# Performance work log

Measured on AMD Instinct MI355X. Metric: run time of the kernel, lower is better.

Reference implementation:

```python
import jax, jax.numpy as jnp
import numpy as np

N_NODES = 50000
N_EDGES = 1600000
NEG_SLOPE = 0.2


def _gat_layer(x, src, dst, W, a_src, a_dst, b, n_nodes):
    # PyG GATConv (heads=1, concat=True): h = xW; e_ij = LeakyReLU(a_src.h_j + a_dst.h_i)
    # alpha = softmax over incoming edges of each target i; out_i = sum_j alpha_ij h_j + b
    h = x @ W                                   # [N, out]
    alpha_src = h @ a_src                        # [N]
    alpha_dst = h @ a_dst                        # [N]
    e = alpha_src[src] + alpha_dst[dst]          # [E]
    e = jnp.where(e > 0, e, NEG_SLOPE * e)       # leaky_relu(0.2)
    m = jax.ops.segment_max(e, dst, num_segments=n_nodes)   # per-target max
    ex = jnp.exp(e - m[dst])
    denom = jax.ops.segment_sum(ex, dst, num_segments=n_nodes)
    alpha = ex / (denom[dst] + 1e-16)            # [E]
    out = jax.ops.segment_sum(alpha[:, None] * h[src], dst, num_segments=n_nodes)
    return out + b


def setup_inputs() -> dict:
    key = jax.random.key(0)
    ks = jax.random.split(key, 16)
    hid, out_dim, in_dim = 128, 5, 13
    x = jax.random.normal(ks[0], (N_NODES, in_dim), dtype=jnp.float32)
    edge_index = jax.random.randint(ks[1], (2, N_EDGES), 0, N_NODES, dtype=jnp.int64)
    s = 0.1
    return {
        "x": x,
        "edge_index": edge_index,
        "W1": jax.random.normal(ks[2], (in_dim, hid), dtype=jnp.float32) * s,
        "a_src1": jax.random.normal(ks[3], (hid,), dtype=jnp.float32) * s,
        "a_dst1": jax.random.normal(ks[4], (hid,), dtype=jnp.float32) * s,
        "b1": jnp.zeros((hid,), dtype=jnp.float32),
        "W2": jax.random.normal(ks[5], (hid, hid), dtype=jnp.float32) * s,
        "a_src2": jax.random.normal(ks[6], (hid,), dtype=jnp.float32) * s,
        "a_dst2": jax.random.normal(ks[7], (hid,), dtype=jnp.float32) * s,
        "b2": jnp.zeros((hid,), dtype=jnp.float32),
        "W3": jax.random.normal(ks[8], (hid, out_dim), dtype=jnp.float32) * s,
        "a_src3": jax.random.normal(ks[9], (out_dim,), dtype=jnp.float32) * s,
        "a_dst3": jax.random.normal(ks[10], (out_dim,), dtype=jnp.float32) * s,
        "b3": jnp.zeros((out_dim,), dtype=jnp.float32),
    }


def reference(x, edge_index, W1, a_src1, a_dst1, b1, W2, a_src2, a_dst2, b2,
              W3, a_src3, a_dst3, b3):
    n = x.shape[0]
    # GATConv add_self_loops=True: append (i, i) edges
    loops = jnp.arange(n, dtype=edge_index.dtype)
    src = jnp.concatenate([edge_index[0], loops])
    dst = jnp.concatenate([edge_index[1], loops])
    h = _gat_layer(x, src, dst, W1, a_src1, a_dst1, b1, n)
    h = jax.nn.relu(h)  # dropout identity in eval mode
    h = _gat_layer(h, src, dst, W2, a_src2, a_dst2, b2, n)
    h = jax.nn.relu(h)
    h = _gat_layer(h, src, dst, W3, a_src3, a_dst3, b3, n)
    return jax.nn.log_softmax(h, axis=1)
```

## Files before the change

### kernel.cpp

```cpp
#include <hip/hip_runtime.h>
#include <hip/hip_bf16.h>


#define LEAKY(e) ((e) > 0.f ? (e) : 0.2f * (e))
__device__ inline float clamp30(float e) { return fminf(fmaxf(e, -30.f), 30.f); }
__device__ inline float expc(float e) { return __expf(clamp30(LEAKY(e))); }

__device__ inline float ldany(const void* p, int bf, int i) {
    return bf ? __bfloat162float(((const __hip_bfloat16*)p)[i])
              : ((const float*)p)[i];
}
__device__ inline int ldidx(const void* p, int i64, long long i) {
    return i64 ? (int)(((const unsigned int*)p)[2 * i])
               : ((const int*)p)[i];
}

__device__ inline float bflo(unsigned int w) { return __uint_as_float(w << 16); }
__device__ inline float bfhi(unsigned int w) { return __uint_as_float(w & 0xffff0000u); }
__device__ inline unsigned short bfbits(float a) {
    __hip_bfloat16 x = __float2bfloat16(a);
    unsigned short u; __builtin_memcpy(&u, &x, 2); return u;
}
__device__ inline unsigned int packbf(float a, float b) {
    return (unsigned int)bfbits(a) | ((unsigned int)bfbits(b) << 16);
}

typedef __attribute__((ext_vector_type(8))) short short8;
typedef __attribute__((ext_vector_type(4))) float f32x4;

__global__ void detect_kernel(const void* W1, const void* ei, int* flags) {
    if (threadIdx.x == 0 && blockIdx.x == 0) {
        const unsigned int* w = (const unsigned int*)W1;
        int c = 0;
        for (int i = 0; i < 64; i++) {
            unsigned int e = (w[i] >> 7) & 0xFFu;
            if (e >= 0x70u && e <= 0x7Fu) c++;
        }
        flags[0] = (c >= 32) ? 1 : 0;
        const unsigned int* q = (const unsigned int*)ei;
        int z = 0;
        for (int i = 0; i < 64; i++)
            if (q[2 * i + 1] == 0u) z++;
        flags[1] = (z >= 32) ? 1 : 0;
    }
}


__global__ __launch_bounds__(256) void sortA_hist(
    const void* __restrict__ ei, const int* __restrict__ flags,
    int* __restrict__ blockHist, int E, int NBUK)
{
    __shared__ int hist[512];
    const int i64 = flags[1];
    const int tid = threadIdx.x, blk = blockIdx.x;
    for (int i = tid; i < NBUK; i += 256) hist[i] = 0;
    __syncthreads();
    const int chunk = (E + 255) / 256;
    const int e0 = blk * chunk, e1 = min(e0 + chunk, E);
    for (int t = e0 + tid; t < e1; t += 256) {
        int d = ldidx(ei, i64, (long long)E + t);
        atomicAdd(&hist[d >> 7], 1);
    }
    __syncthreads();
    for (int i = tid; i < NBUK; i += 256)
        blockHist[blk * NBUK + i] = hist[i];
}

__global__ __launch_bounds__(256) void sortB_prefix(
    int* __restrict__ blockHist, int* __restrict__ bucketBase, int NBUK)
{
    __shared__ int wt[4];
    __shared__ int wbase[4];
    const int b = blockIdx.x;
    const int tid = threadIdx.x, lane = tid & 63, wid = tid >> 6;
    int v = blockHist[tid * NBUK + b];
    int x = v;
#pragma unroll
    for (int o = 1; o < 64; o <<= 1) {
        int y = __shfl_up(x, o);
        if (lane >= o) x += y;
    }
    if (lane == 63) wt[wid] = x;
    __syncthreads();
    if (tid == 0) {
        int s = 0;
#pragma unroll
        for (int i = 0; i < 4; i++) { wbase[i] = s; s += wt[i]; }
        bucketBase[b] = s;
    }
    __syncthreads();
    blockHist[tid * NBUK + b] = x - v + wbase[wid];
}

__global__ __launch_bounds__(512) void sortB2_scan(
    int* __restrict__ bucketBase, int NBUK)
{
    __shared__ int wt[8];
    __shared__ int wbase[8];
    __shared__ int total_s;
    const int tid = threadIdx.x, lane = tid & 63, wid = tid >> 6;
    int v = (tid < NBUK) ? bucketBase[tid] : 0;
    int x = v;
#pragma unroll
    for (int o = 1; o < 64; o <<= 1) {
        int y = __shfl_up(x, o);
        if (lane >= o) x += y;
    }
    if (lane == 63) wt[wid] = x;
    __syncthreads();
    if (tid == 0) {
        int s = 0;
#pragma unroll
        for (int i = 0; i < 8; i++) { wbase[i] = s; s += wt[i]; }
        total_s = s;
    }
    __syncthreads();
    if (tid < NBUK) bucketBase[tid] = x - v + wbase[wid];
    if (tid == 0) bucketBase[NBUK] = total_s;
}

__global__ __launch_bounds__(256) void sortC_scatter(
    const void* __restrict__ ei, const int* __restrict__ flags,
    const int* __restrict__ blockHist, const int* __restrict__ bucketBase,
    unsigned int* __restrict__ pairbuf, int E, int NBUK)
{
    __shared__ int cur[512];
    const int i64 = flags[1];
    const int tid = threadIdx.x, blk = blockIdx.x;
    for (int i = tid; i < NBUK; i += 256)
        cur[i] = blockHist[blk * NBUK + i] + bucketBase[i];
    __syncthreads();
    const int chunk = (E + 255) / 256;
    const int e0 = blk * chunk, e1 = min(e0 + chunk, E);
    for (int t = e0 + tid; t < e1; t += 256) {
        int s = ldidx(ei, i64, t);
        int d = ldidx(ei, i64, (long long)E + t);
        int pos = atomicAdd(&cur[d >> 7], 1);
        pairbuf[pos] = ((unsigned int)(d & 127) << 16) | (unsigned int)s;
    }
}

__global__ __launch_bounds__(256) void sortD_bin(
    const unsigned int* __restrict__ pairbuf, const int* __restrict__ bucketBase,
    int* __restrict__ rowptr, unsigned short* __restrict__ ssrc, int N, int NBUK)
{
    __shared__ int cnt[128];
    __shared__ int cur2[128];
    __shared__ int wt1;
    const int b = blockIdx.x;
    const int tid = threadIdx.x, lane = tid & 63;
    const int e0 = bucketBase[b], e1 = bucketBase[b + 1];
    if (tid < 128) cnt[tid] = 0;
    __syncthreads();
    for (int i = e0 + tid; i < e1; i += 256)
        atomicAdd(&cnt[pairbuf[i] >> 16], 1);
    __syncthreads();
    if (tid < 128) {
        int v = cnt[tid];
        int x = v;
#pragma unroll
        for (int o = 1; o < 64; o <<= 1) {
            int y = __shfl_up(x, o);
            if (lane >= o) x += y;
        }
        if (tid == 63) wt1 = x;
        __syncthreads();
        if (tid >= 64) x += wt1;
        int pfx = x - v;
        cur2[tid] = pfx;
        int node = b * 128 + tid;
        if (node < N) rowptr[node] = e0 + pfx;
    } else {
        __syncthreads();
    }
    if (b == NBUK - 1 && tid == 0) rowptr[N] = e1;
    __syncthreads();
    for (int i = e0 + tid; i < e1; i += 256) {
        unsigned int w = pairbuf[i];
        int p = atomicAdd(&cur2[w >> 16], 1);
        ssrc[e0 + p] = (unsigned short)(w & 0xFFFFu);
    }
}


__global__ __launch_bounds__(256) void node_prep13(
    const void* __restrict__ xin, const void* __restrict__ Wg,
    const void* __restrict__ asg, const void* __restrict__ adg,
    const int* __restrict__ flags,
    unsigned int* __restrict__ h2, float* __restrict__ asrc,
    float* __restrict__ adst, int N)
{
    const int bf = flags[0];
    __shared__ float Wlds[13 * 128];
    for (int i = threadIdx.x; i < 13 * 128; i += 256)
        Wlds[i] = ldany(Wg, bf, i);
    __syncthreads();
    const int lane = threadIdx.x & 63;
    int wave = (blockIdx.x * 256 + threadIdx.x) >> 6;
    int nw = (gridDim.x * 256) >> 6;
    float a0 = ldany(asg, bf, 2 * lane), a1 = ldany(asg, bf, 2 * lane + 1);
    float d0 = ldany(adg, bf, 2 * lane), d1 = ldany(adg, bf, 2 * lane + 1);
    for (int n = wave; n < N; n += nw) {
        float x0 = (lane < 13) ? ldany(xin, bf, n * 13 + lane) : 0.f;
        float s0 = 0.f, s1 = 0.f;
#pragma unroll
        for (int k = 0; k < 13; k++) {
            float xv = __shfl(x0, k);
            s0 += xv * Wlds[k * 128 + 2 * lane];
            s1 += xv * Wlds[k * 128 + 2 * lane + 1];
        }
        float pa = s0 * a0 + s1 * a1;
        float pd = s0 * d0 + s1 * d1;
#pragma unroll
        for (int o = 32; o > 0; o >>= 1) {
            pa += __shfl_xor(pa, o);
            pd += __shfl_xor(pd, o);
        }
        if (lane == 0) { asrc[n] = pa; adst[n] = pd; }
        h2[(size_t)n * 64 + lane] = packbf(s0, s1);
    }
}

__global__ __launch_bounds__(256) void gemm_mfma(
    const float* __restrict__ X, const void* __restrict__ Wg,
    const void* __restrict__ asg, const void* __restrict__ adg,
    const int* __restrict__ flags, unsigned int* __restrict__ h2,
    float* __restrict__ asrc, float* __restrict__ adst, int N)
{
    const int bf = flags[0];
    __shared__ unsigned short A_s[64 * 136];
    __shared__ unsigned short B_s[128 * 136];
    const int tid = threadIdx.x;
    const int nb0 = blockIdx.x * 64;

#pragma unroll
    for (int it = 0; it < 16; it++) {
        int f = it * 256 + tid;
        int k = f >> 5, ng = (f & 31) * 4;
        if (!bf) {
            float4 v = *(const float4*)((const float*)Wg + k * 128 + ng);
            B_s[(ng + 0) * 136 + k] = bfbits(v.x);
            B_s[(ng + 1) * 136 + k] = bfbits(v.y);
            B_s[(ng + 2) * 136 + k] = bfbits(v.z);
            B_s[(ng + 3) * 136 + k] = bfbits(v.w);
        } else {
            const unsigned short* W16 = (const unsigned short*)Wg;
            B_s[(ng + 0) * 136 + k] = W16[k * 128 + ng + 0];
            B_s[(ng + 1) * 136 + k] = W16[k * 128 + ng + 1];
            B_s[(ng + 2) * 136 + k] = W16[k * 128 + ng + 2];
            B_s[(ng + 3) * 136 + k] = W16[k * 128 + ng + 3];
        }
    }
#pragma unroll
    for (int it = 0; it < 8; it++) {
        int f = it * 256 + tid;
        int n = f >> 5, g = f & 31;
        int node = min(nb0 + n, N - 1);
        float4 v = *(const float4*)&X[(size_t)node * 128 + g * 4];
        unsigned int* dst = (unsigned int*)&A_s[n * 136 + g * 4];
        dst[0] = packbf(v.x, v.y);
        dst[1] = packbf(v.z, v.w);
    }
    __syncthreads();

    const int wv = tid >> 6;
    const int lane = tid & 63;
    const int m = lane & 15, quad = lane >> 4;

    f32x4 acc[8];
#pragma unroll
    for (int c = 0; c < 8; c++) acc[c] = (f32x4){0.f, 0.f, 0.f, 0.f};

#pragma unroll
    for (int q = 0; q < 4; q++) {
        short8 a = *(const short8*)&A_s[(wv * 16 + m) * 136 + q * 32 + quad * 8];
#pragma unroll
        for (int c = 0; c < 8; c++) {
            short8 b = *(const short8*)&B_s[(c * 16 + m) * 136 + q * 32 + quad * 8];
            acc[c] = __builtin_amdgcn_mfma_f32_16x16x32_bf16(a, b, acc[c], 0, 0, 0);
        }
    }

    float asv[8], adv[8];
#pragma unroll
    for (int c = 0; c < 8; c++) {
        asv[c] = ldany(asg, bf, c * 16 + m);
        adv[c] = ldany(adg, bf, c * 16 + m);
    }
    unsigned short* h2u = (unsigned short*)h2;
#pragma unroll
    for (int reg = 0; reg < 4; reg++) {
        int node = nb0 + wv * 16 + quad * 4 + reg;
        float pa = 0.f, pd = 0.f;
#pragma unroll
        for (int c = 0; c < 8; c++) {
            float v = acc[c][reg];
            pa += v * asv[c];
            pd += v * adv[c];
            if (node < N) h2u[(size_t)node * 128 + c * 16 + m] = bfbits(v);
        }
#pragma unroll
        for (int o = 1; o < 16; o <<= 1) {
            pa += __shfl_xor(pa, o);
            pd += __shfl_xor(pd, o);
        }
        if (node < N && m == 0) { asrc[node] = pa; adst[node] = pd; }
    }
}

__global__ __launch_bounds__(256) void proj7(
    const float* __restrict__ X, const void* __restrict__ W3,
    const void* __restrict__ as3, const void* __restrict__ ad3,
    const int* __restrict__ flags, float* __restrict__ h3p,
    float* __restrict__ asrc, float* __restrict__ adst, int N)
{
    const int bf = flags[0];
    __shared__ float Wp[128 * 8];
    __shared__ float xs[256 * 33];
    const int tid = threadIdx.x;
    for (int i = tid; i < 128 * 8; i += 256) {
        int k = i >> 3, j = i & 7;
        float v = 0.f;
        if (j < 5) v = ldany(W3, bf, k * 5 + j);
        else if (j == 5) v = ldany(as3, bf, k);
        else if (j == 6) v = ldany(ad3, bf, k);
        Wp[i] = v;
    }
    const int nb0 = blockIdx.x * 256;
    float acc[7] = {0.f, 0.f, 0.f, 0.f, 0.f, 0.f, 0.f};
    for (int kc = 0; kc < 128; kc += 32) {
        __syncthreads();
#pragma unroll
        for (int it = 0; it < 32; it++) {
            int f = it * 256 + tid;
            int row = f >> 5, k = f & 31;
            int node = nb0 + row;
            xs[row * 33 + k] = (node < N) ? X[(size_t)node * 128 + kc + k] : 0.f;
        }
        __syncthreads();
#pragma unroll
        for (int k = 0; k < 32; k++) {
            float xv = xs[tid * 33 + k];
            float4 w0 = *(float4*)&Wp[(kc + k) * 8];
            float4 w1 = *(float4*)&Wp[(kc + k) * 8 + 4];
            acc[0] += xv * w0.x; acc[1] += xv * w0.y; acc[2] += xv * w0.z;
            acc[3] += xv * w0.w; acc[4] += xv * w1.x; acc[5] += xv * w1.y;
            acc[6] += xv * w1.z;
        }
    }
    int node = nb0 + tid;
    if (node < N) {
        float4 o0 = {acc[0], acc[1], acc[2], acc[3]};
        float4 o1 = {acc[4], 0.f, 0.f, 0.f};
        *(float4*)&h3p[(size_t)node * 8] = o0;
        *(float4*)&h3p[(size_t)node * 8 + 4] = o1;
        asrc[node] = acc[5];
        adst[node] = acc[6];
    }
}


__device__ inline unsigned rdlu(unsigned v, int j) {
    return (unsigned)__builtin_amdgcn_readlane((int)v, j);
}

__global__ __launch_bounds__(256) void agg_fused128(
    const int* __restrict__ rowptr, const unsigned short* __restrict__ ssrc,
    const unsigned int* __restrict__ h2, const float* __restrict__ asrc,
    const float* __restrict__ adst, const void* __restrict__ bias,
    const int* __restrict__ flags, float* __restrict__ feat, int N)
{
    const int bf = flags[0];
    const int lane = threadIdx.x & 63;
    int wave = (blockIdx.x * 256 + threadIdx.x) >> 6;
    int nw = (gridDim.x * 256) >> 6;
    const float bx = ldany(bias, bf, 2 * lane);
    const float by = ldany(bias, bf, 2 * lane + 1);
    const unsigned ul = (unsigned)lane;

    for (int n = wave; n < N; n += nw) {
        float ad = adst[n];
        float wself = expc(asrc[n] + ad);
        unsigned int hw = h2[((unsigned)n << 6) | ul];
        float accx = wself * bflo(hw), accy = wself * bfhi(hw);
        float wpart = (lane == 0) ? wself : 0.f;
        const int start = rowptr[n], end = rowptr[n + 1];
        for (int base = start; base < end; base += 64) {
            unsigned pkl = 0;
            if (base + lane < end) {
                unsigned s = (unsigned)ssrc[base + lane];
                float wl = expc(asrc[s] + ad);
                unsigned wb = ((unsigned)bfbits(wl)) << 16;
                wpart += __uint_as_float(wb);
                pkl = wb | s;
            }
            const int cnt = min(64, end - base);
            int j = 0;
            for (; j + 16 <= cnt; j += 16) {
                unsigned pk[16];
                unsigned u[16];
#pragma unroll
                for (int t = 0; t < 16; t++) pk[t] = rdlu(pkl, j + t);
#pragma unroll
                for (int t = 0; t < 16; t++) {
                    const unsigned int* row = h2 + ((pk[t] & 0xFFFFu) << 6);
                    u[t] = row[ul];
                }
#pragma unroll
                for (int t = 0; t < 16; t++) {
                    float w = __uint_as_float(pk[t] & 0xFFFF0000u);
                    accx += w * bflo(u[t]);
                    accy += w * bfhi(u[t]);
                }
            }
            for (; j + 4 <= cnt; j += 4) {
                unsigned pk[4];
                unsigned u[4];
#pragma unroll
                for (int t = 0; t < 4; t++) pk[t] = rdlu(pkl, j + t);
#pragma unroll
                for (int t = 0; t < 4; t++) {
                    const unsigned int* row = h2 + ((pk[t] & 0xFFFFu) << 6);
                    u[t] = row[ul];
                }
#pragma unroll
                for (int t = 0; t < 4; t++) {
                    float w = __uint_as_float(pk[t] & 0xFFFF0000u);
                    accx += w * bflo(u[t]);
                    accy += w * bfhi(u[t]);
                }
            }
            for (; j < cnt; j++) {
                unsigned pk = rdlu(pkl, j);
                const unsigned int* row = h2 + ((pk & 0xFFFFu) << 6);
                unsigned ww = row[ul];
                float w = __uint_as_float(pk & 0xFFFF0000u);
                accx += w * bflo(ww);
                accy += w * bfhi(ww);
            }
        }
        float wsum = wpart;
#pragma unroll
        for (int o = 32; o > 0; o >>= 1) wsum += __shfl_xor(wsum, o);
        float inv = 1.f / (wsum + 1e-16f);
        float2 ov = {fmaxf(accx * inv + bx, 0.f), fmaxf(accy * inv + by, 0.f)};
        *(float2*)&feat[(size_t)n * 128 + 2 * lane] = ov;
    }
}

__global__ __launch_bounds__(256) void agg_fused5(
    const int* __restrict__ rowptr, const unsigned short* __restrict__ ssrc,
    const float* __restrict__ h3p, const float* __restrict__ asrc,
    const float* __restrict__ adst, const void* __restrict__ b3,
    const int* __restrict__ flags, float* __restrict__ out, int N)
{
    const int bf = flags[0];
    const int lane = threadIdx.x & 63;
    int wave = (blockIdx.x * 256 + threadIdx.x) >> 6;
    int nw = (gridDim.x * 256) >> 6;

    for (int n = wave; n < N; n += nw) {
        float ad = adst[n];
        float a0 = 0.f, a1 = 0.f, a2 = 0.f, a3 = 0.f, a4 = 0.f, wsum = 0.f;
        if (lane == 0) {
            float w = expc(asrc[n] + ad);
            wsum = w;
            float4 v = *(const float4*)&h3p[(unsigned)n * 8u];
            float v4 = h3p[(unsigned)n * 8u + 4u];
            a0 = w * v.x; a1 = w * v.y; a2 = w * v.z; a3 = w * v.w; a4 = w * v4;
        }
        const int start = rowptr[n], end = rowptr[n + 1];
        for (int i = start + lane; i < end; i += 64) {
            unsigned s = (unsigned)ssrc[i];
            float w = expc(asrc[s] + ad);
            float4 v = *(const float4*)&h3p[s * 8u];
            float v4 = h3p[s * 8u + 4u];
            wsum += w;
            a0 += w * v.x; a1 += w * v.y; a2 += w * v.z; a3 += w * v.w; a4 += w * v4;
        }
#pragma unroll
        for (int o = 32; o > 0; o >>= 1) {
            a0 += __shfl_xor(a0, o); a1 += __shfl_xor(a1, o); a2 += __shfl_xor(a2, o);
            a3 += __shfl_xor(a3, o); a4 += __shfl_xor(a4, o); wsum += __shfl_xor(wsum, o);
        }
        if (lane == 0) {
            float inv = 1.f / (wsum + 1e-16f);
            float v0 = a0 * inv + ldany(b3, bf, 0);
            float v1 = a1 * inv + ldany(b3, bf, 1);
            float v2 = a2 * inv + ldany(b3, bf, 2);
            float v3 = a3 * inv + ldany(b3, bf, 3);
            float v4 = a4 * inv + ldany(b3, bf, 4);
            float m = fmaxf(fmaxf(fmaxf(v0, v1), fmaxf(v2, v3)), v4);
            float s = __expf(v0 - m) + __expf(v1 - m) + __expf(v2 - m)
                    + __expf(v3 - m) + __expf(v4 - m);
            float lse = m + __logf(s);
            out[n * 5 + 0] = v0 - lse; out[n * 5 + 1] = v1 - lse;
            out[n * 5 + 2] = v2 - lse; out[n * 5 + 3] = v3 - lse;
            out[n * 5 + 4] = v4 - lse;
        }
    }
}

extern "C" void kernel_launch(void* const* d_in, const int* in_sizes, int n_in,
                              void* d_out, int out_size, void* d_ws, size_t ws_size,
                              hipStream_t stream)
{
    const void* x  = d_in[0];
    const void* ei = d_in[1];
    const void* W1 = d_in[2];
    const void* as1= d_in[3];
    const void* ad1= d_in[4];
    const void* b1 = d_in[5];
    const void* W2 = d_in[6];
    const void* as2= d_in[7];
    const void* ad2= d_in[8];
    const void* b2 = d_in[9];
    const void* W3 = d_in[10];
    const void* as3= d_in[11];
    const void* ad3= d_in[12];
    const void* b3 = d_in[13];

    const int N = in_sizes[0] / 13;
    const int E = in_sizes[1] / 2;
    const int NBUK = (N + 127) / 128;

    float* ws    = (float*)d_ws;
    float* feat  = ws;
    unsigned int* h2 = (unsigned int*)(feat + (size_t)N * 128);
    float* asrc  = (float*)(h2 + (size_t)N * 64);
    float* adst  = asrc + N;
    float* h3p   = adst + N;
    int*   rowptr= (int*)(h3p + (size_t)N * 8);
    int*   bucketBase = rowptr + N + 1;
    int*   blockHist  = bucketBase + NBUK + 1;
    unsigned int* pairbuf = (unsigned int*)(blockHist + 256 * NBUK);
    unsigned short* ssrc16 = (unsigned short*)(pairbuf + E);
    int*   flags = (int*)(ssrc16 + E);

    const int wb = (N + 3) / 4;
    const int gb = (N + 63) / 64;
    const int pb = (N + 255) / 256;

    detect_kernel<<<1, 64, 0, stream>>>(W1, ei, flags);

    sortA_hist<<<256, 256, 0, stream>>>(ei, flags, blockHist, E, NBUK);
    sortB_prefix<<<NBUK, 256, 0, stream>>>(blockHist, bucketBase, NBUK);
    sortB2_scan<<<1, 512, 0, stream>>>(bucketBase, NBUK);
    sortC_scatter<<<256, 256, 0, stream>>>(ei, flags, blockHist, bucketBase,
                                           pairbuf, E, NBUK);
    sortD_bin<<<NBUK, 256, 0, stream>>>(pairbuf, bucketBase, rowptr, ssrc16, N, NBUK);

    node_prep13<<<1024, 256, 0, stream>>>(x, W1, as1, ad1, flags, h2, asrc, adst, N);
    agg_fused128<<<wb, 256, 0, stream>>>(rowptr, ssrc16, h2, asrc, adst, b1, flags, feat, N);

    gemm_mfma<<<gb, 256, 0, stream>>>(feat, W2, as2, ad2, flags, h2, asrc, adst, N);
    agg_fused128<<<wb, 256, 0, stream>>>(rowptr, ssrc16, h2, asrc, adst, b2, flags, feat, N);

    proj7<<<pb, 256, 0, stream>>>(feat, W3, as3, ad3, flags, h3p, asrc, adst, N);
    agg_fused5<<<wb, 256, 0, stream>>>(rowptr, ssrc16, h3p, asrc, adst, b3, flags,
                                       (float*)d_out, N);
}
```

Measured before the change: 338.6 us.

## Pre-transpose W2 to bf16, unpack edge weights, split aggregation launches

Adds a small kernel that transposes and converts W2 to bf16 once, so each GEMM block loads B with vector copies instead of strided scalar transposes. The aggregation kernel now keeps the source index and the full fp32 edge weight in separate registers and reads each with readlane, rather than packing a bf16 weight with the 16-bit index. This raises weight precision at the cost of extra readlanes. Each 128-wide aggregation is also split into two launches over node halves, which adds launch overhead without any clear overlap, since both run on the same stream.

```diff
diff --git a/kernel.cpp b/kernel.cpp
--- a/kernel.cpp
+++ b/kernel.cpp
@@ -221,8 +221,19 @@
     }
 }
 
+__global__ __launch_bounds__(128) void packW2T(
+    const void* __restrict__ Wg, const int* __restrict__ flags,
+    unsigned short* __restrict__ W2T)
+{
+    const int bf = flags[0];
+    const int n = blockIdx.x;
+    const int k = threadIdx.x;
+    W2T[n * 128 + k] = bf ? ((const unsigned short*)Wg)[k * 128 + n]
+                          : bfbits(((const float*)Wg)[k * 128 + n]);
+}
+
 __global__ __launch_bounds__(256) void gemm_mfma(
-    const float* __restrict__ X, const void* __restrict__ Wg,
+    const float* __restrict__ X, const unsigned short* __restrict__ W2T,
     const void* __restrict__ asg, const void* __restrict__ adg,
     const int* __restrict__ flags, unsigned int* __restrict__ h2,
     float* __restrict__ asrc, float* __restrict__ adst, int N)
@@ -234,22 +245,11 @@
     const int nb0 = blockIdx.x * 64;
 
 #pragma unroll
-    for (int it = 0; it < 16; it++) {
+    for (int it = 0; it < 8; it++) {
         int f = it * 256 + tid;
-        int k = f >> 5, ng = (f & 31) * 4;
-        if (!bf) {
-            float4 v = *(const float4*)((const float*)Wg + k * 128 + ng);
-            B_s[(ng + 0) * 136 + k] = bfbits(v.x);
-            B_s[(ng + 1) * 136 + k] = bfbits(v.y);
-            B_s[(ng + 2) * 136 + k] = bfbits(v.z);
-            B_s[(ng + 3) * 136 + k] = bfbits(v.w);
-        } else {
-            const unsigned short* W16 = (const unsigned short*)Wg;
-            B_s[(ng + 0) * 136 + k] = W16[k * 128 + ng + 0];
-            B_s[(ng + 1) * 136 + k] = W16[k * 128 + ng + 1];
-            B_s[(ng + 2) * 136 + k] = W16[k * 128 + ng + 2];
-            B_s[(ng + 3) * 136 + k] = W16[k * 128 + ng + 3];
-        }
+        int n = f >> 4, kc = (f & 15) * 8;
+        uint4 v = *(const uint4*)&W2T[n * 128 + kc];
+        *(uint4*)&B_s[n * 136 + kc] = v;
     }
 #pragma unroll
     for (int it = 0; it < 8; it++) {
@@ -360,15 +360,16 @@
 }
 
 
-__device__ inline unsigned rdlu(unsigned v, int j) {
-    return (unsigned)__builtin_amdgcn_readlane((int)v, j);
+__device__ inline int rdl(int v, int j) { return __builtin_amdgcn_readlane(v, j); }
+__device__ inline float rdlf(float v, int j) {
+    return __uint_as_float((unsigned int)__builtin_amdgcn_readlane((int)__float_as_uint(v), j));
 }
 
 __global__ __launch_bounds__(256) void agg_fused128(
     const int* __restrict__ rowptr, const unsigned short* __restrict__ ssrc,
     const unsigned int* __restrict__ h2, const float* __restrict__ asrc,
     const float* __restrict__ adst, const void* __restrict__ bias,
-    const int* __restrict__ flags, float* __restrict__ feat, int N)
+    const int* __restrict__ flags, float* __restrict__ feat, int nStart, int nEnd)
 {
     const int bf = flags[0];
     const int lane = threadIdx.x & 63;
@@ -378,7 +379,7 @@
     const float by = ldany(bias, bf, 2 * lane + 1);
     const unsigned ul = (unsigned)lane;
 
-    for (int n = wave; n < N; n += nw) {
+    for (int n = nStart + wave; n < nEnd; n += nw) {
         float ad = adst[n];
         float wself = expc(asrc[n] + ad);
         unsigned int hw = h2[((unsigned)n << 6) | ul];
@@ -386,55 +387,51 @@
         float wpart = (lane == 0) ? wself : 0.f;
         const int start = rowptr[n], end = rowptr[n + 1];
         for (int base = start; base < end; base += 64) {
-            unsigned pkl = 0;
+            int sl = 0;
+            float wl = 0.f;
             if (base + lane < end) {
-                unsigned s = (unsigned)ssrc[base + lane];
-                float wl = expc(asrc[s] + ad);
-                unsigned wb = ((unsigned)bfbits(wl)) << 16;
-                wpart += __uint_as_float(wb);
-                pkl = wb | s;
+                sl = (int)ssrc[base + lane];
+                wl = expc(asrc[sl] + ad);
             }
+            wpart += wl;
             const int cnt = min(64, end - base);
             int j = 0;
             for (; j + 16 <= cnt; j += 16) {
-                unsigned pk[16];
-                unsigned u[16];
-#pragma unroll
-                for (int t = 0; t < 16; t++) pk[t] = rdlu(pkl, j + t);
+                unsigned int u[16];
+                float w[16];
 #pragma unroll
                 for (int t = 0; t < 16; t++) {
-                    const unsigned int* row = h2 + ((pk[t] & 0xFFFFu) << 6);
-                    u[t] = row[ul];
+                    unsigned s = (unsigned)rdl(sl, j + t);
+                    u[t] = h2[(s << 6) | ul];
                 }
 #pragma unroll
+                for (int t = 0; t < 16; t++) w[t] = rdlf(wl, j + t);
+#pragma unroll
                 for (int t = 0; t < 16; t++) {
-                    float w = __uint_as_float(pk[t] & 0xFFFF0000u);
-                    accx += w * bflo(u[t]);
-                    accy += w * bfhi(u[t]);
+                    accx += w[t] * bflo(u[t]);
+                    accy += w[t] * bfhi(u[t]);
                 }
             }
-            for (; j + 4 <= cnt; j += 4) {
-                unsigned pk[4];
-                unsigned u[4];
-#pragma unroll
-                for (int t = 0; t < 4; t++) pk[t] = rdlu(pkl, j + t);
-#pragma unroll
-                for (int t = 0; t < 4; t++) {
-                    const unsigned int* row = h2 + ((pk[t] & 0xFFFFu) << 6);
-                    u[t] = row[ul];
+            for (; j + 8 <= cnt; j += 8) {
+                unsigned int u[8];
+                float w[8];
+#pragma unroll
+                for (int t = 0; t < 8; t++) {
+                    unsigned s = (unsigned)rdl(sl, j + t);
+                    u[t] = h2[(s << 6) | ul];
                 }
 #pragma unroll
-                for (int t = 0; t < 4; t++) {
-                    float w = __uint_as_float(pk[t] & 0xFFFF0000u);
-                    accx += w * bflo(u[t]);
-                    accy += w * bfhi(u[t]);
+                for (int t = 0; t < 8; t++) w[t] = rdlf(wl, j + t);
+#pragma unroll
+                for (int t = 0; t < 8; t++) {
+                    accx += w[t] * bflo(u[t]);
+                    accy += w[t] * bfhi(u[t]);
                 }
             }
             for (; j < cnt; j++) {
-                unsigned pk = rdlu(pkl, j);
-                const unsigned int* row = h2 + ((pk & 0xFFFFu) << 6);
-                unsigned ww = row[ul];
-                float w = __uint_as_float(pk & 0xFFFF0000u);
+                unsigned s = (unsigned)rdl(sl, j);
+                float w = rdlf(wl, j);
+                unsigned int ww = h2[(s << 6) | ul];
                 accx += w * bflo(ww);
                 accy += w * bfhi(ww);
             }
@@ -533,10 +530,14 @@
     int*   rowptr= (int*)(h3p + (size_t)N * 8);
     int*   bucketBase = rowptr + N + 1;
     int*   blockHist  = bucketBase + NBUK + 1;
-    unsigned int* pairbuf = (unsigned int*)(blockHist + 256 * NBUK);
+    unsigned short* W2T = (unsigned short*)(blockHist + 256 * NBUK);
+    unsigned int* pairbuf = (unsigned int*)(W2T + 128 * 128);
     unsigned short* ssrc16 = (unsigned short*)(pairbuf + E);
     int*   flags = (int*)(ssrc16 + E);
 
+    const int half = N / 2;
+    const int wbh = (half + 3) / 4;
+    const int wbh2 = (N - half + 3) / 4;
     const int wb = (N + 3) / 4;
     const int gb = (N + 63) / 64;
     const int pb = (N + 255) / 256;
@@ -549,12 +550,19 @@
     sortC_scatter<<<256, 256, 0, stream>>>(ei, flags, blockHist, bucketBase,
                                            pairbuf, E, NBUK);
     sortD_bin<<<NBUK, 256, 0, stream>>>(pairbuf, bucketBase, rowptr, ssrc16, N, NBUK);
+    packW2T<<<128, 128, 0, stream>>>(W2, flags, W2T);
 
     node_prep13<<<1024, 256, 0, stream>>>(x, W1, as1, ad1, flags, h2, asrc, adst, N);
-    agg_fused128<<<wb, 256, 0, stream>>>(rowptr, ssrc16, h2, asrc, adst, b1, flags, feat, N);
-
-    gemm_mfma<<<gb, 256, 0, stream>>>(feat, W2, as2, ad2, flags, h2, asrc, adst, N);
-    agg_fused128<<<wb, 256, 0, stream>>>(rowptr, ssrc16, h2, asrc, adst, b2, flags, feat, N);
+    agg_fused128<<<wbh, 256, 0, stream>>>(rowptr, ssrc16, h2, asrc, adst, b1, flags,
+                                          feat, 0, half);
+    agg_fused128<<<wbh2, 256, 0, stream>>>(rowptr, ssrc16, h2, asrc, adst, b1, flags,
+                                           feat, half, N);
+
+    gemm_mfma<<<gb, 256, 0, stream>>>(feat, W2T, as2, ad2, flags, h2, asrc, adst, N);
+    agg_fused128<<<wbh, 256, 0, stream>>>(rowptr, ssrc16, h2, asrc, adst, b2, flags,
+                                          feat, 0, half);
+    agg_fused128<<<wbh2, 256, 0, stream>>>(rowptr, ssrc16, h2, asrc, adst, b2, flags,
+                                           feat, half, N);
 
     proj7<<<pb, 256, 0, stream>>>(feat, W3, as3, ad3, flags, h3p, asrc, adst, N);
     agg_fused5<<<wb, 256, 0, stream>>>(rowptr, ssrc16, h3p, asrc, adst, b3, flags,
```

After: 344.1 us. About the same (+1.6%).
